# Kernel tuning notes

Measured on AMD Instinct MI355X. Metric: run time of the kernel, lower is better.

Reference implementation:

```python
import jax, jax.numpy as jnp
import numpy as np

Q = 10        # icosahedral diamonds
M = 128       # 2**dggrid_level
L = Q * M * M # 163840 icosahedral points
KS = 9        # kernel_size / knn neighbors


def setup_inputs() -> dict:
    key = jax.random.key(0)
    k1, k2, k3, k4 = jax.random.split(key, 4)
    b, c, h, w = 1, 128, 256, 512
    x = jax.random.normal(k1, (b, c, h, w), dtype=jnp.float32)
    codeskmin = jax.random.randint(k2, (L, KS), 0, h * w, dtype=jnp.int32)
    att_w = jax.random.normal(k3, (KS, 2, KS), dtype=jnp.float32) * 0.1
    att_b = jnp.zeros((KS,), dtype=jnp.float32)
    depth_w = jax.random.normal(k4, (c, KS), dtype=jnp.float32) * 0.1
    depth_b = jnp.zeros((c,), dtype=jnp.float32)
    gamma = jnp.ones((c,), dtype=jnp.float32)
    beta = jnp.zeros((c,), dtype=jnp.float32)
    return {"x": x, "codeskmin": codeskmin, "att_w": att_w, "att_b": att_b,
            "depth_w": depth_w, "depth_b": depth_b, "gamma": gamma, "beta": beta}


def reference(x, codeskmin, att_w, att_b, depth_w, depth_b, gamma, beta):
    b, c, h, w = x.shape
    xf = x.reshape(b, c, h * w)
    # KNN gather: (b, c, L, KS)
    xe = xf[:, :, codeskmin]
    # --- SpatialAttentionModule_v1 ---
    avg = jnp.mean(xe, axis=1)           # (b, L, KS)
    mx = jnp.max(xe, axis=1)             # (b, L, KS)
    feat = jnp.stack([avg, mx], axis=1)  # (b, 2, L, KS)
    # Conv2d(2 -> KS, kernel (1,KS), no pad): reduces neighbor axis fully
    att = jnp.einsum('bilk,oik->bol', feat, att_w) + att_b[None, :, None]  # (b, KS, L)
    att = jax.nn.sigmoid(att)
    att = att.transpose(0, 2, 1)[:, None, :, :]  # (b, 1, L, KS)
    xe = att * xe + xe
    # --- depthwise conv over neighbor axis ---
    out = jnp.einsum('bclk,ck->bcl', xe, depth_w) + depth_b[None, :, None]  # (b, c, L)
    # rearrange 'b c (q h w) -> (b q) c h w'
    out = out.reshape(b, c, Q, M, M).transpose(0, 2, 1, 3, 4).reshape(b * Q, c, M, M)
    # BatchNorm (training-mode batch stats)
    mean = jnp.mean(out, axis=(0, 2, 3), keepdims=True)
    var = jnp.var(out, axis=(0, 2, 3), keepdims=True)
    out = (out - mean) * jax.lax.rsqrt(var + 1e-5)
    out = out * gamma[None, :, None, None] + beta[None, :, None, None]
    # Swish
    out = out * jax.nn.sigmoid(out)
    return out
```

## Files before the change

kernel.cpp:

```cpp
#include <hip/hip_runtime.h>
#include <hip/hip_bf16.h>

#define HW 131072
#define NCH 128
#define KS 9
#define L_TOTAL 163840
#define LPW 16

typedef float        f32x2 __attribute__((ext_vector_type(2)));
typedef unsigned int u32x2 __attribute__((ext_vector_type(2)));

static __device__ __forceinline__ float bflo(unsigned int p) { return __uint_as_float(p << 16); }
static __device__ __forceinline__ float bfhi(unsigned int p) { return __uint_as_float(p & 0xffff0000u); }
static __device__ __forceinline__ unsigned short f2bf(float f) {
    unsigned int x = __float_as_uint(f);
    return (unsigned short)((x + 0x7fffu + ((x >> 16) & 1u)) >> 16);
}
static __device__ __forceinline__ unsigned int pack2(float a, float b) {
    return (unsigned int)f2bf(a) | ((unsigned int)f2bf(b) << 16);
}

__global__ __launch_bounds__(256) void transpose_x_kernel(
    const f32x2* __restrict__ xf,
    unsigned int* __restrict__ xT,
    float2* __restrict__ meanmaxP)
{
    __shared__ unsigned short tile[128 * 128];
    __shared__ float ps[4][128];
    __shared__ float pm[4][128];
    const int tid = threadIdx.x;
    const int lane = tid & 63;
    const int wave = tid >> 6;
    const int p0 = blockIdx.x * 128;
    const int pa = 2 * lane, pb = 2 * lane + 1;

    float s0 = 0.f, s1 = 0.f;
    float m0 = -3.4e38f, m1 = -3.4e38f;
    #pragma unroll 8
    for (int it = 0; it < 32; ++it) {
        int c = wave + (it << 2);
        f32x2 v = __builtin_nontemporal_load(&xf[(long)c * (HW / 2) + (p0 >> 1) + lane]);
        tile[pa * 128 + ((c + 2 * pa) & 127)] = f2bf(v.x);
        tile[pb * 128 + ((c + 2 * pb) & 127)] = f2bf(v.y);
        s0 += v.x; s1 += v.y;
        m0 = fmaxf(m0, v.x); m1 = fmaxf(m1, v.y);
    }
    ps[wave][pa] = s0; ps[wave][pb] = s1;
    pm[wave][pa] = m0; pm[wave][pb] = m1;
    __syncthreads();

    #pragma unroll 8
    for (int it = 0; it < 32; ++it) {
        int p = wave + (it << 2);
        int colr = (2 * lane + 2 * p) & 127;
        unsigned int d = *reinterpret_cast<const unsigned int*>(&tile[p * 128 + colr]);
        xT[(long)(p0 + p) * 64 + lane] = d;
    }
    if (tid < 128) {
        float s = ps[0][tid] + ps[1][tid] + ps[2][tid] + ps[3][tid];
        float m = fmaxf(fmaxf(pm[0][tid], pm[1][tid]), fmaxf(pm[2][tid], pm[3][tid]));
        meanmaxP[p0 + tid] = make_float2(s * 0.0078125f, m);
    }
}

__global__ __launch_bounds__(256, 8) void encoder_main_kernel(
    const unsigned int* __restrict__ xT,
    const float2* __restrict__ meanmaxP,
    const int* __restrict__ cks,
    const float* __restrict__ att_w,
    const float* __restrict__ att_b,
    const float* __restrict__ depth_w,
    const float* __restrict__ depth_b,
    unsigned int* __restrict__ ybuf,
    float* __restrict__ gsum, float* __restrict__ gsq)
{
    __shared__ __align__(16) char smem[5312];
    float* attw = (float*)smem;
    float* attb = (float*)(smem + 648);
    int*   lcks = (int*)(smem + 688);
    float* mult = (float*)(smem + 2992);
    float* red  = (float*)smem;

    const int tid = threadIdx.x;
    const int lane = tid & 63;
    const int wave = tid >> 6;
    const int c0 = lane * 2, c1 = c0 + 1;
    const int base_l = blockIdx.x * 64;

    if (tid < 162) attw[tid] = att_w[tid];
    if (tid < KS) attb[tid] = att_b[tid];
    for (int j = tid; j < 64 * KS; j += 256) lcks[j] = cks[base_l * KS + j];

    float dw0[KS], dw1[KS];
    #pragma unroll
    for (int k = 0; k < KS; ++k) {
        dw0[k] = depth_w[c0 * KS + k];
        dw1[k] = depth_w[c1 * KS + k];
    }
    const float db0 = depth_b[c0], db1 = depth_b[c1];
    __syncthreads();

    {
        const int l_local = tid >> 2;
        const int sub = tid & 3;
        if (sub < 3) {
            float mean[KS], mx[KS];
            #pragma unroll
            for (int k = 0; k < KS; ++k) {
                float2 mm = meanmaxP[lcks[l_local * KS + k]];
                mean[k] = mm.x; mx[k] = mm.y;
            }
            #pragma unroll
            for (int oo = 0; oo < 3; ++oo) {
                int o = sub * 3 + oo;
                float logit = attb[o];
                #pragma unroll
                for (int k = 0; k < KS; ++k) {
                    logit = fmaf(mean[k], attw[o * 18 + k], logit);
                    logit = fmaf(mx[k],   attw[o * 18 + 9 + k], logit);
                }
                mult[l_local * KS + o] = 1.0f + 1.0f / (1.0f + __expf(-logit));
            }
        }
    }
    __syncthreads();

    float sum0 = 0.f, sum1 = 0.f, sq0 = 0.f, sq1 = 0.f;
    const int l0 = wave * LPW;

    unsigned int g[2][KS];
    #pragma unroll
    for (int k = 0; k < KS; ++k) {
        int idx = __builtin_amdgcn_readfirstlane(lcks[l0 * KS + k]);
        g[0][k] = xT[(long)idx * 64 + lane];
    }
    #pragma unroll
    for (int k = 0; k < KS; ++k) {
        int idx = __builtin_amdgcn_readfirstlane(lcks[(l0 + 1) * KS + k]);
        g[1][k] = xT[(long)idx * 64 + lane];
    }

    #pragma unroll
    for (int li = 0; li < LPW; ++li) {
        const int l_local = l0 + li;
        float acc0 = db0, acc1 = db1;
        #pragma unroll
        for (int k = 0; k < KS; ++k) {
            unsigned int p = g[li & 1][k];
            float mk = mult[l_local * KS + k];
            acc0 = fmaf(bflo(p) * mk, dw0[k], acc0);
            acc1 = fmaf(bfhi(p) * mk, dw1[k], acc1);
        }
        if (li + 2 < LPW) {
            #pragma unroll
            for (int k = 0; k < KS; ++k) {
                int idx = __builtin_amdgcn_readfirstlane(lcks[(l_local + 2) * KS + k]);
                g[li & 1][k] = xT[(long)idx * 64 + lane];
            }
        }
        __builtin_nontemporal_store(pack2(acc0, acc1),
                                    &ybuf[(long)(base_l + l_local) * 64 + lane]);
        sum0 += acc0; sum1 += acc1;
        sq0 = fmaf(acc0, acc0, sq0);
        sq1 = fmaf(acc1, acc1, sq1);
    }

    __syncthreads();
    red[0 * 256 + tid] = sum0;
    red[1 * 256 + tid] = sum1;
    red[2 * 256 + tid] = sq0;
    red[3 * 256 + tid] = sq1;
    __syncthreads();

    const int grp = tid >> 6;
    const int i = tid & 63;
    float t = red[grp * 256 + i] + red[grp * 256 + 64 + i] +
              red[grp * 256 + 128 + i] + red[grp * 256 + 192 + i];
    float* dst = (grp & 2) ? gsq : gsum;
    atomicAdd(&dst[2 * i + (grp & 1)], t);
}

__global__ __launch_bounds__(256) void finalize_kernel(
    const unsigned int* __restrict__ ybuf,
    const float* __restrict__ gsum, const float* __restrict__ gsq,
    const float* __restrict__ gamma, const float* __restrict__ beta,
    float* __restrict__ out)
{
    __shared__ unsigned short tile[128 * 130];
    const int tid = threadIdx.x;
    const int lane = tid & 63;
    const int wave = tid >> 6;
    const int q = blockIdx.x >> 7;
    const int r0 = (blockIdx.x & 127) * 128;
    const int c0 = 2 * lane, c1 = c0 + 1;

    const long lbase = (long)q * 16384 + r0;
    #pragma unroll 8
    for (int it = 0; it < 32; ++it) {
        int r = wave + (it << 2);
        unsigned int u = __builtin_nontemporal_load(&ybuf[(lbase + r) * 64 + lane]);
        tile[c0 * 130 + r] = (unsigned short)(u & 0xffffu);
        tile[c1 * 130 + r] = (unsigned short)(u >> 16);
    }
    __syncthreads();

    const float invN = 1.0f / (float)L_TOTAL;
    #pragma unroll 4
    for (int it = 0; it < 32; ++it) {
        int c = wave + (it << 2);
        float m = gsum[c] * invN;
        float var = gsq[c] * invN - m * m;
        float sc = gamma[c] * rsqrtf(var + 1e-5f);
        float sh = beta[c] - m * sc;
        unsigned int d = *reinterpret_cast<const unsigned int*>(&tile[c * 130 + 2 * lane]);
        float z0 = fmaf(bflo(d), sc, sh);
        float z1 = fmaf(bfhi(d), sc, sh);
        f32x2 v;
        v.x = z0 / (1.0f + __expf(-z0));
        v.y = z1 / (1.0f + __expf(-z1));
        __builtin_nontemporal_store(v,
            (f32x2*)&out[((long)(q * NCH + c) << 14) + r0 + 2 * lane]);
    }
}

extern "C" void kernel_launch(void* const* d_in, const int* in_sizes, int n_in,
                              void* d_out, int out_size, void* d_ws, size_t ws_size,
                              hipStream_t stream) {
    const f32x2* x_f2  = (const f32x2*)d_in[0];
    const int* cks     = (const int*)d_in[1];
    const float* aw    = (const float*)d_in[2];
    const float* ab    = (const float*)d_in[3];
    const float* dw    = (const float*)d_in[4];
    const float* db    = (const float*)d_in[5];
    const float* gm    = (const float*)d_in[6];
    const float* bt    = (const float*)d_in[7];

    char* ws = (char*)d_ws;
    unsigned int* xT   = (unsigned int*)ws;
    float2* meanmaxP   = (float2*)(ws + 33554432);
    unsigned int* ybuf = (unsigned int*)(ws + 34603008);
    float* gsum        = (float*)(ws + 34603008 + 41943040);
    float* gsq         = gsum + NCH;

    hipMemsetAsync(gsum, 0, 2 * NCH * sizeof(float), stream);

    transpose_x_kernel<<<HW / 128, 256, 0, stream>>>(x_f2, xT, meanmaxP);
    encoder_main_kernel<<<L_TOTAL / 64, 256, 0, stream>>>(
        xT, meanmaxP, cks, aw, ab, dw, db, ybuf, gsum, gsq);
    finalize_kernel<<<1280, 256, 0, stream>>>(
        ybuf, gsum, gsq, gm, bt, (float*)d_out);
}
```

Measured before the change: 338.3 us.

## Replace manual gather double-buffering with scalar-indexed loads and vectorized multiplier reads

Drops the hand-rolled two-deep register prefetch of gathered rows. Each iteration now reads the neighbor indices straight from global memory through a wave-uniform pointer, so they can become scalar loads, and relies on full unrolling to let the compiler schedule the gathers. The attention multipliers are padded to a stride of 12 so they can be read as vector LDS loads. The occupancy hint drops from 8 to 6 and the nontemporal stores become plain stores. The changes aim to cut LDS index traffic and readfirstlane overhead, at the risk of less explicit latency hiding and lower occupancy.

```diff
diff --git a/kernel.cpp b/kernel.cpp
--- a/kernel.cpp
+++ b/kernel.cpp
@@ -8,7 +8,7 @@
 #define LPW 16
 
 typedef float        f32x2 __attribute__((ext_vector_type(2)));
-typedef unsigned int u32x2 __attribute__((ext_vector_type(2)));
+typedef float        f32x4 __attribute__((ext_vector_type(4)));
 
 static __device__ __forceinline__ float bflo(unsigned int p) { return __uint_as_float(p << 16); }
 static __device__ __forceinline__ float bfhi(unsigned int p) { return __uint_as_float(p & 0xffff0000u); }
@@ -63,7 +63,7 @@
     }
 }
 
-__global__ __launch_bounds__(256, 8) void encoder_main_kernel(
+__global__ __launch_bounds__(256, 6) void encoder_main_kernel(
     const unsigned int* __restrict__ xT,
     const float2* __restrict__ meanmaxP,
     const int* __restrict__ cks,
@@ -74,12 +74,12 @@
     unsigned int* __restrict__ ybuf,
     float* __restrict__ gsum, float* __restrict__ gsq)
 {
-    __shared__ __align__(16) char smem[5312];
-    float* attw = (float*)smem;
-    float* attb = (float*)(smem + 648);
-    int*   lcks = (int*)(smem + 688);
-    float* mult = (float*)(smem + 2992);
-    float* red  = (float*)smem;
+    __shared__ __align__(16) char smem[6080];
+    float* attw   = (float*)smem;
+    float* attb   = (float*)(smem + 648);
+    int*   lcks   = (int*)(smem + 688);
+    float* mult12 = (float*)(smem + 2992);
+    float* red    = (float*)smem;
 
     const int tid = threadIdx.x;
     const int lane = tid & 63;
@@ -119,47 +119,44 @@
                     logit = fmaf(mean[k], attw[o * 18 + k], logit);
                     logit = fmaf(mx[k],   attw[o * 18 + 9 + k], logit);
                 }
-                mult[l_local * KS + o] = 1.0f + 1.0f / (1.0f + __expf(-logit));
+                mult12[l_local * 12 + o] = 1.0f + 1.0f / (1.0f + __expf(-logit));
             }
         }
     }
     __syncthreads();
 
     float sum0 = 0.f, sum1 = 0.f, sq0 = 0.f, sq1 = 0.f;
-    const int l0 = wave * LPW;
-
-    unsigned int g[2][KS];
-    #pragma unroll
-    for (int k = 0; k < KS; ++k) {
-        int idx = __builtin_amdgcn_readfirstlane(lcks[l0 * KS + k]);
-        g[0][k] = xT[(long)idx * 64 + lane];
-    }
-    #pragma unroll
-    for (int k = 0; k < KS; ++k) {
-        int idx = __builtin_amdgcn_readfirstlane(lcks[(l0 + 1) * KS + k]);
-        g[1][k] = xT[(long)idx * 64 + lane];
-    }
+    const int lw0 = base_l + wave * LPW;
 
     #pragma unroll
     for (int li = 0; li < LPW; ++li) {
-        const int l_local = l0 + li;
+        const int l = __builtin_amdgcn_readfirstlane(lw0 + li);
+        const int* ckp = cks + (long)l * KS;
+        int idx[KS];
+        #pragma unroll
+        for (int k = 0; k < KS; ++k) idx[k] = ckp[k];
+
+        unsigned int pv[KS];
+        #pragma unroll
+        for (int k = 0; k < KS; ++k) {
+            const unsigned int* rowp = xT + ((long)idx[k] << 6);
+            pv[k] = rowp[lane];
+        }
+
+        const int ll = wave * LPW + li;
+        f32x4 mA = *(const f32x4*)&mult12[ll * 12 + 0];
+        f32x4 mB = *(const f32x4*)&mult12[ll * 12 + 4];
+        float m8 = mult12[ll * 12 + 8];
+        float mk[KS] = {mA.x, mA.y, mA.z, mA.w, mB.x, mB.y, mB.z, mB.w, m8};
+
         float acc0 = db0, acc1 = db1;
         #pragma unroll
         for (int k = 0; k < KS; ++k) {
-            unsigned int p = g[li & 1][k];
-            float mk = mult[l_local * KS + k];
-            acc0 = fmaf(bflo(p) * mk, dw0[k], acc0);
-            acc1 = fmaf(bfhi(p) * mk, dw1[k], acc1);
+            acc0 = fmaf(bflo(pv[k]) * mk[k], dw0[k], acc0);
+            acc1 = fmaf(bfhi(pv[k]) * mk[k], dw1[k], acc1);
         }
-        if (li + 2 < LPW) {
-            #pragma unroll
-            for (int k = 0; k < KS; ++k) {
-                int idx = __builtin_amdgcn_readfirstlane(lcks[(l_local + 2) * KS + k]);
-                g[li & 1][k] = xT[(long)idx * 64 + lane];
-            }
-        }
-        __builtin_nontemporal_store(pack2(acc0, acc1),
-                                    &ybuf[(long)(base_l + l_local) * 64 + lane]);
+
+        ybuf[(long)l * 64 + lane] = pack2(acc0, acc1);
         sum0 += acc0; sum1 += acc1;
         sq0 = fmaf(acc0, acc0, sq0);
         sq1 = fmaf(acc1, acc1, sq1);
@@ -218,8 +215,7 @@
         f32x2 v;
         v.x = z0 / (1.0f + __expf(-z0));
         v.y = z1 / (1.0f + __expf(-z1));
-        __builtin_nontemporal_store(v,
-            (f32x2*)&out[((long)(q * NCH + c) << 14) + r0 + 2 * lane]);
+        *(f32x2*)&out[((long)(q * NCH + c) << 14) + r0 + 2 * lane] = v;
     }
 }
 
```

Result: faster. 319.1 us (-5.7%).
